# Kernel optimization log

Hardware: AMD Instinct MI355X
Metric: run time of the kernel (lower is better)

The kernel has to match this reference:

```python
import jax, jax.numpy as jnp
import numpy as np

LN_EPS = 1e-5
NEG_INF = -1e30


def setup_inputs() -> dict:
    key = jax.random.key(0)
    k1, k2, k3 = jax.random.split(key, 3)
    B, N, D = 8192, 64, 64
    fi = jax.random.normal(k1, (B, N, D), dtype=jnp.float32)
    # orthogonal-init correlation matrix (matches nn.init.orthogonal_)
    a = jax.random.normal(k2, (D, D), dtype=jnp.float32)
    q, r = jnp.linalg.qr(a)
    correlation_mat = q * jnp.sign(jnp.diag(r))[None, :]
    ln1_gamma = jnp.ones((D,), dtype=jnp.float32)
    ln1_beta = jnp.zeros((D,), dtype=jnp.float32)
    last_w = jax.random.normal(k3, (1, 2 * D), dtype=jnp.float32) * 0.05
    last_b = jnp.zeros((1,), dtype=jnp.float32)
    return {"fi": fi, "correlation_mat": correlation_mat,
            "ln1_gamma": ln1_gamma, "ln1_beta": ln1_beta,
            "last_w": last_w, "last_b": last_b}


def _layer_norm(x, gamma, beta):
    mu = jnp.mean(x, axis=-1, keepdims=True)
    var = jnp.mean(jnp.square(x - mu), axis=-1, keepdims=True)
    return (x - mu) * jax.lax.rsqrt(var + LN_EPS) * gamma + beta


def reference(fi, correlation_mat, ln1_gamma, ln1_beta, last_w, last_b):
    B, N, D = fi.shape
    # pairwise bilinear scores: beta[b,i,j] = fi[b,i] @ C @ fi[b,j]
    fiC = jnp.einsum('bid,de->bie', fi, correlation_mat)        # [B,N,D]
    beta = jnp.einsum('bie,bje->bij', fiC, fi)                  # [B,N,N]
    # exclude self (i==j), matching the Python loop which skips j==i
    diag_mask = jnp.eye(N, dtype=bool)
    beta = jnp.where(diag_mask[None, :, :], NEG_INF, beta)
    alpha = jax.nn.softmax(beta, axis=-1)                       # [B,N,N]
    vi = jnp.einsum('bij,bjd->bid', alpha, fi)                  # [B,N,D]
    vi = jax.nn.relu(_layer_norm(vi, ln1_gamma, ln1_beta))
    all_inputs = jnp.concatenate([fi, vi], axis=-1)             # [B,N,2D]
    weight = jax.nn.sigmoid(jnp.einsum('bnk,ok->bno', all_inputs, last_w) + last_b)
    return weight  # [B, N, 1]
```

## Files before the change

kernel.cpp:

```cpp
#include <hip/hip_runtime.h>
#include <hip/hip_bf16.h>

typedef __attribute__((ext_vector_type(8))) short short8;
typedef __attribute__((ext_vector_type(4))) float floatx4;

constexpr float LN_EPS = 1e-5f;
constexpr float NEG_INF_V = -1e30f;

__device__ unsigned short g_wsC[8192];

__device__ __forceinline__ unsigned short bf16hi_sw(float x) {
    unsigned int u = __builtin_bit_cast(unsigned int, x);
    u += 0x7FFFu + ((u >> 16) & 1u);
    return (unsigned short)(u >> 16);
}
__device__ __forceinline__ float bf16f(unsigned short h) {
    unsigned int u = ((unsigned int)h) << 16;
    return __builtin_bit_cast(float, u);
}
__device__ __forceinline__ unsigned int pk2(float a, float b) {
    float2 f2; f2.x = a; f2.y = b;
    __hip_bfloat162 h2 = __float22bfloat162_rn(f2);
    unsigned int u;
    __builtin_memcpy(&u, &h2, sizeof(u));
    return u;
}
__device__ __forceinline__ void splitpk(float a, float b,
                                        unsigned int& H, unsigned int& L) {
    H = pk2(a, b);
    const float ha = __builtin_bit_cast(float, H << 16);
    const float hb = __builtin_bit_cast(float, H & 0xFFFF0000u);
    L = pk2(a - ha, b - hb);
}

__device__ __forceinline__ unsigned int permlo(unsigned int A, unsigned int B) {
    return __builtin_amdgcn_perm(B, A, 0x05040100u);
}
__device__ __forceinline__ unsigned int permhi(unsigned int A, unsigned int B) {
    return __builtin_amdgcn_perm(B, A, 0x07060302u);
}

template<int CTRL>
__device__ __forceinline__ float dppadd(float v) {
    int t = __builtin_amdgcn_update_dpp(0, __builtin_bit_cast(int, v),
                                        CTRL, 0xF, 0xF, true);
    return v + __builtin_bit_cast(float, t);
}
template<int CTRL>
__device__ __forceinline__ float dppmax(float v) {
    int t = __builtin_amdgcn_update_dpp(0, __builtin_bit_cast(int, v),
                                        CTRL, 0xF, 0xF, true);
    return fmaxf(v, __builtin_bit_cast(float, t));
}
__device__ __forceinline__ float rsum16(float v) {
    v = dppadd<0x121>(v); v = dppadd<0x122>(v);
    v = dppadd<0x124>(v); v = dppadd<0x128>(v);
    return v;
}
__device__ __forceinline__ float rmax16(float v) {
    v = dppmax<0x121>(v); v = dppmax<0x122>(v);
    v = dppmax<0x124>(v); v = dppmax<0x128>(v);
    return v;
}

__device__ __forceinline__ int eoff(int r, int c) {
    return r * 64 + ((((c >> 3) ^ r) & 7) << 3) + (c & 7);
}
__device__ __forceinline__ int goff(int r, int g) {
    return r * 64 + (((g ^ r) & 7) << 3);
}
__device__ __forceinline__ int moff(int r, int c) {
    return r * 32 + ((((c >> 3) ^ (r >> 2)) & 3) << 3) + (c & 7);
}
__device__ __forceinline__ int aoff(int r, int c) {
    return r * 64 + ((((c >> 3) ^ (r >> 2)) & 7) << 3) + (c & 7);
}

__global__ void prep_corr(const float* __restrict__ corr) {
    const int tid  = threadIdx.x;
    const int lane = tid & 63;
    const int t    = tid >> 6;
    const int nn   = lane & 15;
    const int q    = lane >> 4;
    const int brow = 16 * t + nn;
    #pragma unroll
    for (int kk = 0; kk < 2; ++kk) {
        const int kbase = (kk * 4 + q) * 8;
        short8 H8, L8;
        #pragma unroll
        for (int e = 0; e < 8; ++e) {
            const float v = corr[(kbase + e) * 64 + brow];
            const unsigned short hh = bf16hi_sw(v);
            const unsigned short ll = bf16hi_sw(v - bf16f(hh));
            H8[e] = (short)hh;
            L8[e] = (short)ll;
        }
        const int idx = ((t * 2 + kk) * 64 + lane) * 8;
        *(short8*)&g_wsC[idx]        = H8;
        *(short8*)&g_wsC[4096 + idx] = L8;
    }
}

__global__ __launch_bounds__(256, 5)
void attn_mfma(const float* __restrict__ fi,
               const float* __restrict__ ln_g,
               const float* __restrict__ ln_b,
               const float* __restrict__ lw,
               const float* __restrict__ lb,
               float* __restrict__ out)
{
    __shared__ __align__(16) unsigned short sFiH[4096], sFiL[4096];
    __shared__ __align__(16) unsigned short sFtH[4096];
    __shared__ __align__(16) unsigned short sM[4096];

    const int tid  = threadIdx.x;
    const int lane = tid & 63;
    const int w    = tid >> 6;
    const int n    = lane & 15;
    const int quad = lane >> 4;
    const size_t blk = blockIdx.x;

    unsigned short* mW = &sM[w * 1024];

    const short8* wCH = (const short8*)g_wsC;
    const short8* wCL = (const short8*)(g_wsC + 4096);

    const int C = 4 * n;
    const int R = 4 * (tid >> 4);
    float d0v[4];
    {
        const float* fb = fi + blk * 4096;
        float4 v[4];
        #pragma unroll
        for (int i = 0; i < 4; ++i)
            v[i] = *(const float4*)(fb + (R + i) * 64 + C);

        const float4 w0v = *(const float4*)&lw[C];
        #pragma unroll
        for (int i = 0; i < 4; ++i) {
            float p = v[i].x * w0v.x + v[i].y * w0v.y
                    + v[i].z * w0v.z + v[i].w * w0v.w;
            d0v[i] = rsum16(p);
        }

        unsigned int H01[4], H23[4], L01[4], L23[4];
        #pragma unroll
        for (int i = 0; i < 4; ++i) {
            splitpk(v[i].x, v[i].y, H01[i], L01[i]);
            splitpk(v[i].z, v[i].w, H23[i], L23[i]);
        }
        #pragma unroll
        for (int i = 0; i < 4; ++i) {
            uint2 H = {H01[i], H23[i]};
            uint2 L = {L01[i], L23[i]};
            *(uint2*)&sFiH[eoff(R + i, C)] = H;
            *(uint2*)&sFiL[eoff(R + i, C)] = L;
        }
        uint2 t0 = {permlo(H01[0], H01[1]), permlo(H01[2], H01[3])};
        uint2 t1 = {permhi(H01[0], H01[1]), permhi(H01[2], H01[3])};
        uint2 t2 = {permlo(H23[0], H23[1]), permlo(H23[2], H23[3])};
        uint2 t3 = {permhi(H23[0], H23[1]), permhi(H23[2], H23[3])};
        *(uint2*)&sFtH[eoff(C + 0, R)] = t0;
        *(uint2*)&sFtH[eoff(C + 1, R)] = t1;
        *(uint2*)&sFtH[eoff(C + 2, R)] = t2;
        *(uint2*)&sFtH[eoff(C + 3, R)] = t3;
    }

    const int arow = 16 * w + n;

    short8 Ah[2], Al[2];
    #pragma unroll
    for (int kk = 0; kk < 2; ++kk) {
        Ah[kk] = *(const short8*)&sFiH[goff(arow, kk * 4 + quad)];
        Al[kk] = *(const short8*)&sFiL[goff(arow, kk * 4 + quad)];
    }
    floatx4 acc1[4];
    #pragma unroll
    for (int t = 0; t < 4; ++t) {
        floatx4 acc = {0.f, 0.f, 0.f, 0.f};
        #pragma unroll
        for (int kk = 0; kk < 2; ++kk) {
            const int f = t * 2 + kk;
            short8 bh = wCH[f * 64 + lane];
            short8 bl = wCL[f * 64 + lane];
            acc = __builtin_amdgcn_mfma_f32_16x16x32_bf16(Ah[kk], bh, acc, 0, 0, 0);
            acc = __builtin_amdgcn_mfma_f32_16x16x32_bf16(Al[kk], bh, acc, 0, 0, 0);
            acc = __builtin_amdgcn_mfma_f32_16x16x32_bf16(Ah[kk], bl, acc, 0, 0, 0);
        }
        acc1[t] = acc;
    }

    __syncthreads();

    floatx4 acc2[4];
    #pragma unroll
    for (int t = 0; t < 4; ++t) acc2[t] = floatx4{0.f, 0.f, 0.f, 0.f};

    #pragma unroll
    for (int kh = 0; kh < 2; ++kh) {
        #pragma unroll
        for (int th = 0; th < 2; ++th) {
            const int t = 2 * kh + th;
            unsigned int H01, L01, H23, L23;
            splitpk(acc1[t][0], acc1[t][1], H01, L01);
            splitpk(acc1[t][2], acc1[t][3], H23, L23);
            const int c  = 16 * th + n;
            const int r0 = 4 * quad;
            mW[moff(r0 + 0, c)]       = (unsigned short)H01;
            mW[moff(r0 + 1, c)]       = (unsigned short)(H01 >> 16);
            mW[moff(r0 + 2, c)]       = (unsigned short)H23;
            mW[moff(r0 + 3, c)]       = (unsigned short)(H23 >> 16);
            mW[512 + moff(r0 + 0, c)] = (unsigned short)L01;
            mW[512 + moff(r0 + 1, c)] = (unsigned short)(L01 >> 16);
            mW[512 + moff(r0 + 2, c)] = (unsigned short)L23;
            mW[512 + moff(r0 + 3, c)] = (unsigned short)(L23 >> 16);
        }
        short8 PAh = *(const short8*)&mW[moff(n, quad * 8)];
        short8 PAl = *(const short8*)&mW[512 + moff(n, quad * 8)];
        #pragma unroll
        for (int t = 0; t < 4; ++t) {
            const int brow = 16 * t + n;
            short8 bh = *(const short8*)&sFiH[goff(brow, kh * 4 + quad)];
            short8 bl = *(const short8*)&sFiL[goff(brow, kh * 4 + quad)];
            acc2[t] = __builtin_amdgcn_mfma_f32_16x16x32_bf16(PAh, bh, acc2[t], 0, 0, 0);
            acc2[t] = __builtin_amdgcn_mfma_f32_16x16x32_bf16(PAl, bh, acc2[t], 0, 0, 0);
            acc2[t] = __builtin_amdgcn_mfma_f32_16x16x32_bf16(PAh, bl, acc2[t], 0, 0, 0);
        }
    }

    #pragma unroll
    for (int reg = 0; reg < 4; ++reg) {
        const int row = 16 * w + quad * 4 + reg;
        float x[4];
        #pragma unroll
        for (int t = 0; t < 4; ++t) {
            x[t] = acc2[t][reg];
            if (row == 16 * t + n) x[t] = NEG_INF_V;
        }
        float m = fmaxf(fmaxf(x[0], x[1]), fmaxf(x[2], x[3]));
        m = rmax16(m);
        #pragma unroll
        for (int t = 0; t < 4; ++t) x[t] = __expf(x[t] - m);
        const unsigned int A01 = pk2(x[0], x[1]);
        const unsigned int A23 = pk2(x[2], x[3]);
        const int lr = quad * 4 + reg;
        mW[aoff(lr, 0 + n)]  = (unsigned short)A01;
        mW[aoff(lr, 16 + n)] = (unsigned short)(A01 >> 16);
        mW[aoff(lr, 32 + n)] = (unsigned short)A23;
        mW[aoff(lr, 48 + n)] = (unsigned short)(A23 >> 16);
    }

    short8 AAh[2];
    #pragma unroll
    for (int kk = 0; kk < 2; ++kk)
        AAh[kk] = *(const short8*)&mW[aoff(n, (kk * 4 + quad) * 8)];
    floatx4 acc3[4];
    #pragma unroll
    for (int t = 0; t < 4; ++t) {
        floatx4 acc = {0.f, 0.f, 0.f, 0.f};
        const int brow = 16 * t + n;
        #pragma unroll
        for (int kk = 0; kk < 2; ++kk) {
            short8 bh = *(const short8*)&sFtH[goff(brow, kk * 4 + quad)];
            acc = __builtin_amdgcn_mfma_f32_16x16x32_bf16(AAh[kk], bh, acc, 0, 0, 0);
        }
        acc3[t] = acc;
    }

    float gv[4], bv[4], w1v[4];
    #pragma unroll
    for (int t = 0; t < 4; ++t) {
        gv[t]  = ln_g[16 * t + n];
        bv[t]  = ln_b[16 * t + n];
        w1v[t] = lw[64 + 16 * t + n];
    }
    const float bias = lb[0];
    float res[4];
    #pragma unroll
    for (int reg = 0; reg < 4; ++reg) {
        float s  = acc3[0][reg] + acc3[1][reg] + acc3[2][reg] + acc3[3][reg];
        float s2 = acc3[0][reg] * acc3[0][reg] + acc3[1][reg] * acc3[1][reg]
                 + acc3[2][reg] * acc3[2][reg] + acc3[3][reg] * acc3[3][reg];
        s  = rsum16(s);
        s2 = rsum16(s2);
        const float mu  = s * (1.0f / 64.0f);
        const float var = s2 * (1.0f / 64.0f) - mu * mu;
        const float rstd = __builtin_amdgcn_rsqf(var + LN_EPS);
        float dotp = 0.f;
        #pragma unroll
        for (int t = 0; t < 4; ++t) {
            float lnv = (acc3[t][reg] - mu) * rstd * gv[t] + bv[t];
            lnv = fmaxf(lnv, 0.f);
            dotp += lnv * w1v[t];
        }
        dotp = rsum16(dotp);
        res[reg] = __builtin_amdgcn_rcpf(1.0f + __expf(-(dotp + d0v[reg] + bias)));
    }
    if (n == 0) {
        float4 o = {res[0], res[1], res[2], res[3]};
        *(float4*)&out[blk * 64 + 16 * w + quad * 4] = o;
    }
}

extern "C" void kernel_launch(void* const* d_in, const int* in_sizes, int n_in,
                              void* d_out, int out_size, void* d_ws, size_t ws_size,
                              hipStream_t stream) {
    const float* fi   = (const float*)d_in[0];
    const float* corr = (const float*)d_in[1];
    const float* g    = (const float*)d_in[2];
    const float* b    = (const float*)d_in[3];
    const float* lw   = (const float*)d_in[4];
    const float* lb   = (const float*)d_in[5];
    float* out        = (float*)d_out;

    const int B = in_sizes[0] / 4096;
    hipLaunchKernelGGL(prep_corr, dim3(1), dim3(256), 0, stream, corr);
    hipLaunchKernelGGL(attn_mfma, dim3(B), dim3(256), 0, stream,
                       fi, g, b, lw, lb, out);
}
```

Baseline: 214.8 us.

## Compute fi·w0 dot via MFMA, double-buffer P tiles, simplify diag mask

The fi·w0 projection now runs as split-bf16 MFMAs against a padded weight tile prepared in the prep kernel, replacing per-lane FMAs and a 16-lane reduction. Both halves of the per-wave P tile are written to a doubled LDS scratch area before the second GEMM, so there is no interleaved write/read per k-half. The diagonal mask uses a wave-uniform index. LDS per block grows and launch bounds drop from 5 to 4 blocks per CU, which lowers occupancy.

```diff
diff --git a/kernel.cpp b/kernel.cpp
--- a/kernel.cpp
+++ b/kernel.cpp
@@ -7,7 +7,7 @@
 constexpr float LN_EPS = 1e-5f;
 constexpr float NEG_INF_V = -1e30f;
 
-__device__ unsigned short g_wsC[8192];
+__device__ unsigned short g_wsC[10240];
 
 __device__ __forceinline__ unsigned short bf16hi_sw(float x) {
     unsigned int u = __builtin_bit_cast(unsigned int, x);
@@ -76,7 +76,8 @@
     return r * 64 + ((((c >> 3) ^ (r >> 2)) & 7) << 3) + (c & 7);
 }
 
-__global__ void prep_corr(const float* __restrict__ corr) {
+__global__ void prep_corr(const float* __restrict__ corr,
+                          const float* __restrict__ lw) {
     const int tid  = threadIdx.x;
     const int lane = tid & 63;
     const int t    = tid >> 6;
@@ -99,9 +100,26 @@
         *(short8*)&g_wsC[idx]        = H8;
         *(short8*)&g_wsC[4096 + idx] = L8;
     }
-}
-
-__global__ __launch_bounds__(256, 5)
+    if (t == 0) {
+        #pragma unroll
+        for (int kk = 0; kk < 2; ++kk) {
+            short8 H8, L8;
+            #pragma unroll
+            for (int e = 0; e < 8; ++e) {
+                const float v = (nn == 0) ? lw[(kk * 4 + q) * 8 + e] : 0.0f;
+                const unsigned short hh = bf16hi_sw(v);
+                const unsigned short ll = bf16hi_sw(v - bf16f(hh));
+                H8[e] = (short)hh;
+                L8[e] = (short)ll;
+            }
+            const int idx = (kk * 64 + lane) * 8;
+            *(short8*)&g_wsC[8192 + idx] = H8;
+            *(short8*)&g_wsC[9216 + idx] = L8;
+        }
+    }
+}
+
+__global__ __launch_bounds__(256, 4)
 void attn_mfma(const float* __restrict__ fi,
                const float* __restrict__ ln_g,
                const float* __restrict__ ln_b,
@@ -111,7 +129,7 @@
 {
     __shared__ __align__(16) unsigned short sFiH[4096], sFiL[4096];
     __shared__ __align__(16) unsigned short sFtH[4096];
-    __shared__ __align__(16) unsigned short sM[4096];
+    __shared__ __align__(16) unsigned short sM[8192];
 
     const int tid  = threadIdx.x;
     const int lane = tid & 63;
@@ -119,29 +137,18 @@
     const int n    = lane & 15;
     const int quad = lane >> 4;
     const size_t blk = blockIdx.x;
-
-    unsigned short* mW = &sM[w * 1024];
-
-    const short8* wCH = (const short8*)g_wsC;
-    const short8* wCL = (const short8*)(g_wsC + 4096);
+    const int rw   = __builtin_amdgcn_readfirstlane(w);
+
+    unsigned short* mW = &sM[w * 2048];
 
     const int C = 4 * n;
     const int R = 4 * (tid >> 4);
-    float d0v[4];
     {
         const float* fb = fi + blk * 4096;
         float4 v[4];
         #pragma unroll
         for (int i = 0; i < 4; ++i)
             v[i] = *(const float4*)(fb + (R + i) * 64 + C);
-
-        const float4 w0v = *(const float4*)&lw[C];
-        #pragma unroll
-        for (int i = 0; i < 4; ++i) {
-            float p = v[i].x * w0v.x + v[i].y * w0v.y
-                    + v[i].z * w0v.z + v[i].w * w0v.w;
-            d0v[i] = rsum16(p);
-        }
 
         unsigned int H01[4], H23[4], L01[4], L23[4];
         #pragma unroll
@@ -181,20 +188,25 @@
         #pragma unroll
         for (int kk = 0; kk < 2; ++kk) {
             const int f = t * 2 + kk;
-            short8 bh = wCH[f * 64 + lane];
-            short8 bl = wCL[f * 64 + lane];
+            short8 bh = *(const short8*)&g_wsC[(f * 64 + lane) * 8];
+            short8 bl = *(const short8*)&g_wsC[4096 + (f * 64 + lane) * 8];
             acc = __builtin_amdgcn_mfma_f32_16x16x32_bf16(Ah[kk], bh, acc, 0, 0, 0);
             acc = __builtin_amdgcn_mfma_f32_16x16x32_bf16(Al[kk], bh, acc, 0, 0, 0);
             acc = __builtin_amdgcn_mfma_f32_16x16x32_bf16(Ah[kk], bl, acc, 0, 0, 0);
         }
         acc1[t] = acc;
     }
+    floatx4 accd = {0.f, 0.f, 0.f, 0.f};
+    #pragma unroll
+    for (int kk = 0; kk < 2; ++kk) {
+        short8 bh = *(const short8*)&g_wsC[8192 + (kk * 64 + lane) * 8];
+        short8 bl = *(const short8*)&g_wsC[9216 + (kk * 64 + lane) * 8];
+        accd = __builtin_amdgcn_mfma_f32_16x16x32_bf16(Ah[kk], bh, accd, 0, 0, 0);
+        accd = __builtin_amdgcn_mfma_f32_16x16x32_bf16(Al[kk], bh, accd, 0, 0, 0);
+        accd = __builtin_amdgcn_mfma_f32_16x16x32_bf16(Ah[kk], bl, accd, 0, 0, 0);
+    }
 
     __syncthreads();
-
-    floatx4 acc2[4];
-    #pragma unroll
-    for (int t = 0; t < 4; ++t) acc2[t] = floatx4{0.f, 0.f, 0.f, 0.f};
 
     #pragma unroll
     for (int kh = 0; kh < 2; ++kh) {
@@ -206,37 +218,48 @@
             splitpk(acc1[t][2], acc1[t][3], H23, L23);
             const int c  = 16 * th + n;
             const int r0 = 4 * quad;
-            mW[moff(r0 + 0, c)]       = (unsigned short)H01;
-            mW[moff(r0 + 1, c)]       = (unsigned short)(H01 >> 16);
-            mW[moff(r0 + 2, c)]       = (unsigned short)H23;
-            mW[moff(r0 + 3, c)]       = (unsigned short)(H23 >> 16);
-            mW[512 + moff(r0 + 0, c)] = (unsigned short)L01;
-            mW[512 + moff(r0 + 1, c)] = (unsigned short)(L01 >> 16);
-            mW[512 + moff(r0 + 2, c)] = (unsigned short)L23;
-            mW[512 + moff(r0 + 3, c)] = (unsigned short)(L23 >> 16);
-        }
-        short8 PAh = *(const short8*)&mW[moff(n, quad * 8)];
-        short8 PAl = *(const short8*)&mW[512 + moff(n, quad * 8)];
+            unsigned short* m = &mW[kh * 1024];
+            m[moff(r0 + 0, c)]       = (unsigned short)H01;
+            m[moff(r0 + 1, c)]       = (unsigned short)(H01 >> 16);
+            m[moff(r0 + 2, c)]       = (unsigned short)H23;
+            m[moff(r0 + 3, c)]       = (unsigned short)(H23 >> 16);
+            m[512 + moff(r0 + 0, c)] = (unsigned short)L01;
+            m[512 + moff(r0 + 1, c)] = (unsigned short)(L01 >> 16);
+            m[512 + moff(r0 + 2, c)] = (unsigned short)L23;
+            m[512 + moff(r0 + 3, c)] = (unsigned short)(L23 >> 16);
+        }
+    }
+    short8 PAh[2], PAl[2];
+    #pragma unroll
+    for (int kh = 0; kh < 2; ++kh) {
+        PAh[kh] = *(const short8*)&mW[kh * 1024 + moff(n, quad * 8)];
+        PAl[kh] = *(const short8*)&mW[kh * 1024 + 512 + moff(n, quad * 8)];
+    }
+    floatx4 acc2[4];
+    #pragma unroll
+    for (int t = 0; t < 4; ++t) acc2[t] = floatx4{0.f, 0.f, 0.f, 0.f};
+    #pragma unroll
+    for (int kh = 0; kh < 2; ++kh) {
         #pragma unroll
         for (int t = 0; t < 4; ++t) {
             const int brow = 16 * t + n;
             short8 bh = *(const short8*)&sFiH[goff(brow, kh * 4 + quad)];
             short8 bl = *(const short8*)&sFiL[goff(brow, kh * 4 + quad)];
-            acc2[t] = __builtin_amdgcn_mfma_f32_16x16x32_bf16(PAh, bh, acc2[t], 0, 0, 0);
-            acc2[t] = __builtin_amdgcn_mfma_f32_16x16x32_bf16(PAl, bh, acc2[t], 0, 0, 0);
-            acc2[t] = __builtin_amdgcn_mfma_f32_16x16x32_bf16(PAh, bl, acc2[t], 0, 0, 0);
+            acc2[t] = __builtin_amdgcn_mfma_f32_16x16x32_bf16(PAh[kh], bh, acc2[t], 0, 0, 0);
+            acc2[t] = __builtin_amdgcn_mfma_f32_16x16x32_bf16(PAl[kh], bh, acc2[t], 0, 0, 0);
+            acc2[t] = __builtin_amdgcn_mfma_f32_16x16x32_bf16(PAh[kh], bl, acc2[t], 0, 0, 0);
         }
     }
 
     #pragma unroll
     for (int reg = 0; reg < 4; ++reg) {
-        const int row = 16 * w + quad * 4 + reg;
         float x[4];
         #pragma unroll
-        for (int t = 0; t < 4; ++t) {
-            x[t] = acc2[t][reg];
-            if (row == 16 * t + n) x[t] = NEG_INF_V;
-        }
+        for (int t = 0; t < 4; ++t) x[t] = acc2[t][reg];
+        #pragma unroll
+        for (int t = 0; t < 4; ++t)
+            if (t == rw)
+                x[t] = (n == 4 * quad + reg) ? NEG_INF_V : x[t];
         float m = fmaxf(fmaxf(x[0], x[1]), fmaxf(x[2], x[3]));
         m = rmax16(m);
         #pragma unroll
@@ -294,7 +317,7 @@
             dotp += lnv * w1v[t];
         }
         dotp = rsum16(dotp);
-        res[reg] = __builtin_amdgcn_rcpf(1.0f + __expf(-(dotp + d0v[reg] + bias)));
+        res[reg] = __builtin_amdgcn_rcpf(1.0f + __expf(-(dotp + accd[reg] + bias)));
     }
     if (n == 0) {
         float4 o = {res[0], res[1], res[2], res[3]};
@@ -314,7 +337,7 @@
     float* out        = (float*)d_out;
 
     const int B = in_sizes[0] / 4096;
-    hipLaunchKernelGGL(prep_corr, dim3(1), dim3(256), 0, stream, corr);
+    hipLaunchKernelGGL(prep_corr, dim3(1), dim3(256), 0, stream, corr, lw);
     hipLaunchKernelGGL(attn_mfma, dim3(B), dim3(256), 0, stream,
                        fi, g, b, lw, lb, out);
 }
```

New measurement: 216.6 us. Within noise of the previous version (+0.8%).
